# Kernel tuning notes

Measured on AMD Instinct MI355X. Metric: run time of the kernel, lower is better.

The kernel has to match this reference:

```python
import jax, jax.numpy as jnp
import numpy as np


def setup_inputs() -> dict:
    key = jax.random.key(0)
    k1, k2, k3, k4, k5 = jax.random.split(key, 5)
    B, S, D, F, E = 4, 4096, 1024, 2048, 8
    top_k = 2
    num_tokens = B * S
    capacity = max(int(num_tokens / E * 1.25), 4)  # 2560
    scale = 0.02
    return {
        "x": jax.random.normal(k1, (B, S, D), dtype=jnp.float32),
        "gate_w": jax.random.normal(k2, (D, E), dtype=jnp.float32) * scale,
        "w_gate": jax.random.normal(k3, (E, D, F), dtype=jnp.float32) * scale,
        "w_up": jax.random.normal(k4, (E, D, F), dtype=jnp.float32) * scale,
        "w_down": jax.random.normal(k5, (E, F, D), dtype=jnp.float32) * scale,
        "num_experts": E,
        "top_k": top_k,
        "capacity": capacity,
    }


AUX_LOSS_WEIGHT = 0.01


def reference(x, gate_w, w_gate, w_up, w_down, num_experts, top_k, capacity):
    B, S, D = x.shape
    N = B * S
    x_flat = x.reshape(N, D)

    # ---- Router ----
    logits = x_flat @ gate_w                      # [N, E]
    probs = jax.nn.softmax(logits, axis=-1)
    weights, indices = jax.lax.top_k(probs, top_k)  # [N, K]
    weights = weights / jnp.sum(weights, axis=-1, keepdims=True)

    # ---- Capacity-based dispatch ----
    indices_flat = indices.reshape(-1)            # [N*K]
    x_rep = jnp.repeat(x_flat, top_k, axis=0)     # [N*K, D]
    expert_mask = jax.nn.one_hot(indices_flat, num_experts, dtype=jnp.int32)  # [N*K, E]
    token_priority = jnp.cumsum(expert_mask, axis=0) * expert_mask
    token_rank = jnp.sum(token_priority, axis=1)  # [N*K], 1-based rank within expert
    valid = (token_rank > 0) & (token_rank <= capacity)
    gather_idx = indices_flat * capacity + (token_rank - 1)  # [N*K]

    total_slots = num_experts * capacity
    # drop-mode scatter: invalid rows are sent out-of-bounds and dropped
    safe_idx = jnp.where(valid, gather_idx, total_slots)
    dispatched = jnp.zeros((total_slots, D), dtype=x.dtype)
    dispatched = dispatched.at[safe_idx].set(x_rep, mode="drop")
    dispatched = dispatched.reshape(num_experts, capacity, D)  # [E, C, D]

    # ---- Fused experts (grouped BMM, SwiGLU) ----
    gate = jnp.einsum("ecd,edf->ecf", dispatched, w_gate)
    up = jnp.einsum("ecd,edf->ecf", dispatched, w_up)
    hidden = jax.nn.silu(gate) * up
    expert_out = jnp.einsum("ecf,efd->ecd", hidden, w_down)
    expert_out_flat = expert_out.reshape(total_slots, D)

    # ---- Combine (row-aligned gather; dropped tokens contribute zero) ----
    gathered = expert_out_flat[jnp.clip(gather_idx, 0, total_slots - 1)]
    combined = jnp.where(valid[:, None], gathered, jnp.zeros((), dtype=x.dtype))
    combined = combined.reshape(N, top_k, D)
    output = jnp.sum(combined * weights[:, :, None], axis=1)  # [N, D]

    # ---- Aux load-balance loss ----
    mask = jax.nn.one_hot(indices, num_experts, dtype=jnp.float32).sum(axis=1)  # [N, E]
    f = mask.sum(axis=0) / (N * top_k + 1e-9)
    P = probs.mean(axis=0)
    aux_loss = num_experts * jnp.sum(f * P) * AUX_LOSS_WEIGHT

    return output.reshape(B, S, D), aux_loss
```

## Files before the change

### kernel.cpp

```cpp
#include <hip/hip_runtime.h>
#include <stdint.h>

#define N_TOK 16384
#define DIM   1024
#define NEXP  8
#define FF    2048
#define CAP   2560
#define NSLOT (NEXP*CAP)

using f32x4  = __attribute__((ext_vector_type(4))) float;
using bf16x8 = __attribute__((ext_vector_type(8))) short;

__device__ __forceinline__ unsigned short f2bf(float f){
  union { float f; unsigned u; } c; c.f = f;
  unsigned u = c.u + 0x7FFFu + ((c.u >> 16) & 1u);
  return (unsigned short)(u >> 16);
}
__device__ __forceinline__ float bf2f(unsigned short h){
  union { unsigned u; float f; } c; c.u = ((unsigned)h) << 16; return c.f;
}

__device__ __forceinline__ void gld16(const unsigned short* g, unsigned short* l){
  __builtin_amdgcn_global_load_lds((__attribute__((address_space(1))) void*)(void*)g,
                                   (__attribute__((address_space(3))) void*)l,
                                   16, 0, 0);
}

#define HBAR __builtin_amdgcn_s_barrier()
#define LG0  asm volatile("s_waitcnt lgkmcnt(0)" ::: "memory")

__global__ __launch_bounds__(256) void k_router(
    const float* __restrict__ x, const float* __restrict__ gate_w,
    float* __restrict__ probs, int* __restrict__ topidx, float* __restrict__ topw)
{
  __shared__ float gwT[NEXP][DIM];
  int tid = threadIdx.x;
  for (int i = tid; i < DIM*NEXP; i += 256) gwT[i & 7][i >> 3] = gate_w[i];
  __syncthreads();
  int wave = tid >> 6, lane = tid & 63;
  int t = blockIdx.x * 4 + wave;
  const float* xr = x + (size_t)t * DIM;
  double acc[NEXP];
  #pragma unroll
  for (int e = 0; e < NEXP; e++) acc[e] = 0.0;
  for (int j = 0; j < DIM/64; j++){
    double xv = (double)xr[lane + 64*j];
    #pragma unroll
    for (int e = 0; e < NEXP; e++) acc[e] += xv * (double)gwT[e][lane + 64*j];
  }
  #pragma unroll
  for (int off = 32; off >= 1; off >>= 1){
    #pragma unroll
    for (int e = 0; e < NEXP; e++) acc[e] += __shfl_xor(acc[e], off, 64);
  }
  if (lane == 0){
    double m = acc[0];
    #pragma unroll
    for (int e = 1; e < NEXP; e++) m = fmax(m, acc[e]);
    double p[NEXP], Z = 0.0;
    #pragma unroll
    for (int e = 0; e < NEXP; e++){ p[e] = exp(acc[e] - m); Z += p[e]; }
    double invZ = 1.0 / Z;
    #pragma unroll
    for (int e = 0; e < NEXP; e++){ p[e] *= invZ; probs[t*NEXP + e] = (float)p[e]; }
    int i0 = 0; double p0 = p[0];
    #pragma unroll
    for (int e = 1; e < NEXP; e++) if (p[e] > p0){ p0 = p[e]; i0 = e; }
    int i1 = (i0 == 0) ? 1 : 0; double p1 = p[i1];
    #pragma unroll
    for (int e = 0; e < NEXP; e++) if (e != i0 && p[e] > p1){ p1 = p[e]; i1 = e; }
    double s = p0 + p1;
    topidx[t*2+0] = i0; topidx[t*2+1] = i1;
    topw [t*2+0] = (float)(p0/s); topw[t*2+1] = (float)(p1/s);
  }
}

__global__ __launch_bounds__(1024) void k_scan(
    const int* __restrict__ topidx,
    int* __restrict__ slot_token, int* __restrict__ tok_slots,
    int* __restrict__ counts_total)
{
  __shared__ int sc[1024][NEXP];
  const int t = threadIdx.x;
  const int base_i = t * 32;
  int ids[32];
  #pragma unroll
  for (int j = 0; j < 32; j++) ids[j] = topidx[base_i + j];
  int b[NEXP];
  #pragma unroll
  for (int e = 0; e < NEXP; e++) b[e] = 0;
  #pragma unroll
  for (int j = 0; j < 32; j++){
    #pragma unroll
    for (int e = 0; e < NEXP; e++) if (ids[j] == e) b[e]++;
  }
  #pragma unroll
  for (int e = 0; e < NEXP; e++) sc[t][e] = b[e];
  __syncthreads();
  for (int off = 1; off < 1024; off <<= 1){
    int tmp[NEXP];
    #pragma unroll
    for (int e = 0; e < NEXP; e++) tmp[e] = (t >= off) ? sc[t-off][e] : 0;
    __syncthreads();
    #pragma unroll
    for (int e = 0; e < NEXP; e++) sc[t][e] += tmp[e];
    __syncthreads();
  }
  int myb[NEXP];
  #pragma unroll
  for (int e = 0; e < NEXP; e++) myb[e] = sc[t][e] - b[e];
  if (t == 1023){
    #pragma unroll
    for (int e = 0; e < NEXP; e++) counts_total[e] = sc[1023][e];
  }
  #pragma unroll
  for (int j = 0; j < 32; j++){
    int slot = -1;
    #pragma unroll
    for (int e = 0; e < NEXP; e++){
      if (ids[j] == e){
        int r = myb[e]; myb[e] = r + 1;
        if (r < CAP){
          slot = e*CAP + r;
          slot_token[slot] = (base_i + j) >> 1;
        }
      }
    }
    tok_slots[base_i + j] = slot;
  }
}

template<int MODE>
__global__ __launch_bounds__(256) void k_tcv(
    const float* __restrict__ in, unsigned short* __restrict__ out,
    int R, int C, size_t estride)
{
  __shared__ float tt[64][65];
  const int e  = blockIdx.z;
  const float* ine = in + (size_t)e * R * C;
  unsigned short* oute = out + (size_t)e * estride;
  const int c0 = blockIdx.x * 64, r0 = blockIdx.y * 64;
  const int tid = threadIdx.x;
  #pragma unroll
  for (int i = 0; i < 4; i++){
    int idx = i*256 + tid;
    int row = idx >> 4, c4 = idx & 15;
    float4 v = *(const float4*)(ine + (size_t)(r0 + row)*C + c0 + c4*4);
    tt[c4*4+0][row] = v.x; tt[c4*4+1][row] = v.y;
    tt[c4*4+2][row] = v.z; tt[c4*4+3][row] = v.w;
  }
  __syncthreads();
  #pragma unroll
  for (int i = 0; i < 2; i++){
    int cl = i*32 + (tid >> 3);
    int rs = (tid & 7) * 8;
    int c  = c0 + cl;
    int orow = (MODE == 0) ? ((c>>4)*32 + (c&15))
             : (MODE == 1) ? ((c>>4)*32 + 16 + (c&15))
             : c;
    unsigned long long pk0 = 0, pk1 = 0;
    #pragma unroll
    for (int j = 0; j < 4; j++) pk0 |= (unsigned long long)f2bf(tt[cl][rs+j]) << (16*j);
    #pragma unroll
    for (int j = 0; j < 4; j++) pk1 |= (unsigned long long)f2bf(tt[cl][rs+4+j]) << (16*j);
    unsigned long long* dst = (unsigned long long*)(oute + (size_t)orow*R + r0 + rs);
    dst[0] = pk0; dst[1] = pk1;
  }
}

__global__ __launch_bounds__(256) void k_gather(
    const float* __restrict__ x, const int* __restrict__ slot_token,
    unsigned short* __restrict__ disp)
{
  const int s = blockIdx.x;
  const int t = slot_token[s];
  const int tid = threadIdx.x;
  unsigned long long pk = 0ull;
  if (t >= 0){
    float4 v = *(const float4*)(x + (size_t)t*DIM + tid*4);
    pk =  (unsigned long long)f2bf(v.x)
       | ((unsigned long long)f2bf(v.y) << 16)
       | ((unsigned long long)f2bf(v.z) << 32)
       | ((unsigned long long)f2bf(v.w) << 48);
  }
  *(unsigned long long*)(disp + (size_t)s*DIM + tid*4) = pk;
}

__device__ __forceinline__ void stg(const unsigned short* gsrc, int ldg,
                                    unsigned short* Lh, int wave, int lane){
  const int sl = (lane & 3) ^ ((lane >> 3) & 3);
  #pragma unroll
  for (int j = 0; j < 2; j++){
    int bi = wave*2 + j;
    gld16(gsrc + (size_t)(bi*16 + (lane >> 2))*ldg + sl*8, Lh + bi*512);
  }
}
__device__ __forceinline__ bf16x8 frd(const unsigned short* Lh, int r, int g){
  return *(const bf16x8*)(Lh + r*32 + (((g ^ ((r >> 1) & 3))) << 3));
}
template<int MG>
__device__ __forceinline__ void mm16(f32x4 (&acc)[8][4], const bf16x8 (&a)[4], const bf16x8 (&b)[4]){
  #pragma unroll
  for (int i = 0; i < 4; i++)
    #pragma unroll
    for (int n = 0; n < 4; n++)
      acc[MG*4+i][n] = __builtin_amdgcn_mfma_f32_16x16x32_bf16(a[i], b[n], acc[MG*4+i][n], 0, 0, 0);
}

#define HALF_STEP(RS, DOSTG, VMW, ASRC, BSRC)                                   \
  {                                                                             \
    unsigned short* LA = lds + (RS)*16384;                                      \
    unsigned short* LB = LA + 8192;                                             \
    unsigned short* NS = lds + (((RS)+3)&3)*16384;                              \
    bf16x8 a[4], b[4];                                                          \
    _Pragma("unroll")                                                           \
    for (int i = 0; i < 4; i++) a[i] = frd(LA, wr*128 + i*16 + l15, g);         \
    _Pragma("unroll")                                                           \
    for (int n = 0; n < 4; n++) b[n] = frd(LB, wc*64 + n*16 + l15, g);          \
    if (DOSTG) stg(ASRC, LDG, NS, wave, lane);                                  \
    HBAR; LG0;                                                                  \
    __builtin_amdgcn_s_setprio(1);  mm16<0>(acc, a, b);                         \
    __builtin_amdgcn_s_setprio(0);                                              \
    HBAR;                                                                       \
    _Pragma("unroll")                                                           \
    for (int i = 0; i < 4; i++) a[i] = frd(LA, wr*128 + (4+i)*16 + l15, g);     \
    if (DOSTG) stg(BSRC, LDG, NS + 8192, wave, lane);                           \
    HBAR; LG0;                                                                  \
    __builtin_amdgcn_s_setprio(1);  mm16<1>(acc, a, b);                         \
    __builtin_amdgcn_s_setprio(0);                                              \
    if ((VMW) == 4) { asm volatile("s_waitcnt vmcnt(4)" ::: "memory"); }        \
    else if ((VMW) == 0) { asm volatile("s_waitcnt vmcnt(0)" ::: "memory"); }   \
    HBAR;                                                                       \
  }

template<int KDIM, int LDG, int EPI>
__global__ __launch_bounds__(512, 2) void k_gemm8(
    const unsigned short* __restrict__ A,
    const unsigned short* __restrict__ B,
    unsigned short* __restrict__ Out0,
    unsigned short* __restrict__ Out1)
{
  constexpr int NH    = KDIM / 32;
  constexpr int BROWS = (EPI == 1) ? 2*FF : DIM;
  constexpr int LDO   = (EPI == 1) ? FF : DIM;
  __shared__ unsigned short lds[65536];
  const int id = blockIdx.x;
  const int e  = id & 7;
  int t  = id >> 3;
  int ks = 0;
  if (EPI == 2){ ks = t & 1; t >>= 1; }
  const int mt = t % 10, nt = t / 10;
  const int m0 = mt*256, n0 = nt*256;
  const unsigned short* Ab = A + ((size_t)e*CAP   + m0) * LDG + (size_t)ks*KDIM;
  const unsigned short* Bb = B + ((size_t)e*BROWS + n0) * LDG + (size_t)ks*KDIM;
  const int tid = threadIdx.x, wave = tid >> 6, lane = tid & 63;
  const int wr = wave >> 2, wc = wave & 3;
  const int g = lane >> 4, l15 = lane & 15;

  f32x4 acc[8][4];
  const f32x4 z4 = {0.f,0.f,0.f,0.f};
  #pragma unroll
  for (int i = 0; i < 8; i++)
    #pragma unroll
    for (int n = 0; n < 4; n++) acc[i][n] = z4;

  stg(Ab,      LDG, lds + 0*16384,        wave, lane);
  stg(Bb,      LDG, lds + 0*16384 + 8192, wave, lane);
  stg(Ab + 32, LDG, lds + 1*16384,        wave, lane);
  stg(Bb + 32, LDG, lds + 1*16384 + 8192, wave, lane);
  stg(Ab + 64, LDG, lds + 2*16384,        wave, lane);
  stg(Bb + 64, LDG, lds + 2*16384 + 8192, wave, lane);
  asm volatile("s_waitcnt vmcnt(4)" ::: "memory");
  HBAR;

  for (int h = 0; h + 8 <= NH; h += 4){
    HALF_STEP(0, true, -1, Ab + (size_t)(h+3)*32, Bb + (size_t)(h+3)*32);
    HALF_STEP(1, true,  4, Ab + (size_t)(h+4)*32, Bb + (size_t)(h+4)*32);
    HALF_STEP(2, true, -1, Ab + (size_t)(h+5)*32, Bb + (size_t)(h+5)*32);
    HALF_STEP(3, true,  4, Ab + (size_t)(h+6)*32, Bb + (size_t)(h+6)*32);
  }
  HALF_STEP(0, true, -1, Ab + (size_t)(NH-1)*32, Bb + (size_t)(NH-1)*32);
  HALF_STEP(1, false, 0, Ab, Bb);
  HALF_STEP(2, false, -1, Ab, Bb);
  HALF_STEP(3, false, -1, Ab, Bb);

  if (EPI == 1){
    unsigned short* H = Out0 + ((size_t)e*CAP + m0 + wr*128) * (size_t)LDO;
    const int hc0 = (n0 + wc*64) >> 1;
    #pragma unroll
    for (int mf = 0; mf < 8; mf++)
      #pragma unroll
      for (int q = 0; q < 4; q++){
        int r = mf*16 + g*4 + q;
        #pragma unroll
        for (int p = 0; p < 2; p++){
          float gg = acc[mf][2*p][q], uu = acc[mf][2*p+1][q];
          float h = gg / (1.f + __expf(-gg)) * uu;
          H[(size_t)r*LDO + hc0 + p*16 + l15] = f2bf(h);
        }
      }
  } else {
    unsigned short* P = (ks ? Out1 : Out0);
    unsigned short* O = P + ((size_t)e*CAP + m0 + wr*128) * (size_t)LDO + n0 + wc*64;
    #pragma unroll
    for (int mf = 0; mf < 8; mf++)
      #pragma unroll
      for (int q = 0; q < 4; q++){
        int r = mf*16 + g*4 + q;
        #pragma unroll
        for (int n = 0; n < 4; n++)
          O[(size_t)r*LDO + n*16 + l15] = f2bf(acc[mf][n][q]);
      }
  }
}

__global__ __launch_bounds__(256) void k_combine(
    const unsigned short* __restrict__ P0, const unsigned short* __restrict__ P1,
    const int* __restrict__ tok_slots, const float* __restrict__ topw,
    float* __restrict__ out)
{
  const int t = blockIdx.x*2 + (threadIdx.x >> 7);
  const int tid = threadIdx.x & 127;
  const int s0 = tok_slots[t*2+0], s1 = tok_slots[t*2+1];
  const float w0 = topw[t*2+0], w1 = topw[t*2+1];
  float r[8];
  #pragma unroll
  for (int j = 0; j < 8; j++) r[j] = 0.f;
  if (s0 >= 0){
    bf16x8 v0 = *(const bf16x8*)(P0 + (size_t)s0*DIM + tid*8);
    bf16x8 v1 = *(const bf16x8*)(P1 + (size_t)s0*DIM + tid*8);
    #pragma unroll
    for (int j = 0; j < 8; j++)
      r[j] += w0 * (bf2f((unsigned short)v0[j]) + bf2f((unsigned short)v1[j]));
  }
  if (s1 >= 0){
    bf16x8 v0 = *(const bf16x8*)(P0 + (size_t)s1*DIM + tid*8);
    bf16x8 v1 = *(const bf16x8*)(P1 + (size_t)s1*DIM + tid*8);
    #pragma unroll
    for (int j = 0; j < 8; j++)
      r[j] += w1 * (bf2f((unsigned short)v0[j]) + bf2f((unsigned short)v1[j]));
  }
  float4* o = (float4*)(out + (size_t)t*DIM + tid*8);
  o[0] = make_float4(r[0], r[1], r[2], r[3]);
  o[1] = make_float4(r[4], r[5], r[6], r[7]);
}

__global__ __launch_bounds__(256) void k_aux(
    const float* __restrict__ probs, const int* __restrict__ counts_total,
    float* __restrict__ aux_out)
{
  const int tid = threadIdx.x;
  float pe[NEXP];
  #pragma unroll
  for (int e = 0; e < NEXP; e++) pe[e] = 0.f;
  for (int i = tid; i < N_TOK; i += 256){
    #pragma unroll
    for (int e = 0; e < NEXP; e++) pe[e] += probs[i*NEXP + e];
  }
  #pragma unroll
  for (int off = 32; off >= 1; off >>= 1){
    #pragma unroll
    for (int e = 0; e < NEXP; e++) pe[e] += __shfl_xor(pe[e], off, 64);
  }
  __shared__ float part[4][NEXP];
  const int wave = tid >> 6, lane = tid & 63;
  if (lane == 0){
    #pragma unroll
    for (int e = 0; e < NEXP; e++) part[wave][e] = pe[e];
  }
  __syncthreads();
  if (tid == 0){
    float aux = 0.f;
    for (int e = 0; e < NEXP; e++){
      float P = (part[0][e] + part[1][e] + part[2][e] + part[3][e]) / (float)N_TOK;
      float f = (float)counts_total[e] / ((float)(N_TOK*2) + 1e-9f);
      aux += f * P;
    }
    aux_out[0] = (float)NEXP * aux * 0.01f;
  }
}

extern "C" void kernel_launch(void* const* d_in, const int* in_sizes, int n_in,
                              void* d_out, int out_size, void* d_ws, size_t ws_size,
                              hipStream_t stream)
{
  const float* x      = (const float*)d_in[0];
  const float* gate_w = (const float*)d_in[1];
  const float* w_gate = (const float*)d_in[2];
  const float* w_up   = (const float*)d_in[3];
  const float* w_down = (const float*)d_in[4];
  float* out = (float*)d_out;

  uint8_t* ws = (uint8_t*)d_ws;
  float* probs        = (float*)ws;             ws += (size_t)N_TOK*NEXP*4;
  int*   topidx       = (int*)ws;               ws += (size_t)N_TOK*2*4;
  float* topw         = (float*)ws;             ws += (size_t)N_TOK*2*4;
  int*   slot_token   = (int*)ws;               ws += (size_t)NSLOT*4;
  int*   tok_slots    = (int*)ws;               ws += (size_t)N_TOK*2*4;
  int*   counts_total = (int*)ws;               ws += 256;
  unsigned short* disp   = (unsigned short*)ws; ws += (size_t)NSLOT*DIM*2;
  unsigned short* hidden = (unsigned short*)ws; ws += (size_t)NSLOT*FF*2;
  unsigned short* B1     = (unsigned short*)ws; ws += (size_t)NEXP*2*FF*DIM*2;
  unsigned short* wdT    = (unsigned short*)ws; ws += (size_t)NEXP*DIM*FF*2;
  size_t need = (size_t)(ws - (uint8_t*)d_ws);
  if (ws_size < need) return;
  unsigned short* P0 = disp;
  unsigned short* P1 = B1;

  hipMemsetAsync(slot_token, 0xFF, (size_t)NSLOT * sizeof(int), stream);

  k_router<<<N_TOK/4, 256, 0, stream>>>(x, gate_w, probs, topidx, topw);
  k_scan<<<1, 1024, 0, stream>>>(topidx, slot_token, tok_slots, counts_total);
  k_tcv<0><<<dim3(FF/64, DIM/64, NEXP), 256, 0, stream>>>(w_gate, B1, DIM, FF, (size_t)2*FF*DIM);
  k_tcv<1><<<dim3(FF/64, DIM/64, NEXP), 256, 0, stream>>>(w_up,   B1, DIM, FF, (size_t)2*FF*DIM);
  k_tcv<2><<<dim3(DIM/64, FF/64, NEXP), 256, 0, stream>>>(w_down, wdT, FF, DIM, (size_t)DIM*FF);
  k_gather<<<NSLOT, 256, 0, stream>>>(x, slot_token, disp);
  k_gemm8<DIM, DIM, 1><<<1280, 512, 0, stream>>>(disp, B1, hidden, nullptr);
  k_gemm8<DIM, FF, 2><<<640, 512, 0, stream>>>(hidden, wdT, P0, P1);
  k_combine<<<N_TOK/2, 256, 0, stream>>>(P0, P1, tok_slots, topw, out);
  k_aux<<<1, 256, 0, stream>>>(probs, counts_total, out + (size_t)N_TOK*DIM);
}
```

Measured before the change: 501.6 us.

## Restructure GEMM main loop, merge weight-convert launches, fold aux loss into scan

Replaces the unrolled HALF_STEP GEMM pipeline with a per-stage loop. Each iteration issues both A and B prefetches, reads the whole A fragment set and prefetches the next stage's B fragments, then runs all 32 MFMAs per stage with fewer barriers. It also merges the three weight transpose/convert launches into one grid and moves the aux-loss reduction into the scan kernel, removing a launch. The fewer barriers and larger MFMA bursts may raise register pressure or change how well loads overlap with compute.

Result: faster. 483.4 us (-3.6%).

```diff
diff --git a/kernel.cpp b/kernel.cpp
--- a/kernel.cpp
+++ b/kernel.cpp
@@ -28,6 +28,7 @@
 
 #define HBAR __builtin_amdgcn_s_barrier()
 #define LG0  asm volatile("s_waitcnt lgkmcnt(0)" ::: "memory")
+#define SBAR0 __builtin_amdgcn_sched_barrier(0)
 
 __global__ __launch_bounds__(256) void k_router(
     const float* __restrict__ x, const float* __restrict__ gate_w,
@@ -76,9 +77,9 @@
 }
 
 __global__ __launch_bounds__(1024) void k_scan(
-    const int* __restrict__ topidx,
+    const int* __restrict__ topidx, const float* __restrict__ probs,
     int* __restrict__ slot_token, int* __restrict__ tok_slots,
-    int* __restrict__ counts_total)
+    float* __restrict__ aux_out)
 {
   __shared__ int sc[1024][NEXP];
   const int t = threadIdx.x;
@@ -109,10 +110,9 @@
   int myb[NEXP];
   #pragma unroll
   for (int e = 0; e < NEXP; e++) myb[e] = sc[t][e] - b[e];
-  if (t == 1023){
-    #pragma unroll
-    for (int e = 0; e < NEXP; e++) counts_total[e] = sc[1023][e];
-  }
+  int cnt[NEXP];
+  #pragma unroll
+  for (int e = 0; e < NEXP; e++) cnt[e] = sc[1023][e];
   #pragma unroll
   for (int j = 0; j < 32; j++){
     int slot = -1;
@@ -128,24 +128,66 @@
     }
     tok_slots[base_i + j] = slot;
   }
-}
-
-template<int MODE>
-__global__ __launch_bounds__(256) void k_tcv(
-    const float* __restrict__ in, unsigned short* __restrict__ out,
-    int R, int C, size_t estride)
+  __syncthreads();
+  float pe[NEXP];
+  #pragma unroll
+  for (int e = 0; e < NEXP; e++) pe[e] = 0.f;
+  for (int i = t; i < N_TOK; i += 1024){
+    const float4* pr = (const float4*)(probs + i*NEXP);
+    float4 v0 = pr[0], v1 = pr[1];
+    pe[0] += v0.x; pe[1] += v0.y; pe[2] += v0.z; pe[3] += v0.w;
+    pe[4] += v1.x; pe[5] += v1.y; pe[6] += v1.z; pe[7] += v1.w;
+  }
+  #pragma unroll
+  for (int off = 32; off >= 1; off >>= 1){
+    #pragma unroll
+    for (int e = 0; e < NEXP; e++) pe[e] += __shfl_xor(pe[e], off, 64);
+  }
+  __syncthreads();
+  float* scf = (float*)&sc[0][0];
+  const int wv = t >> 6, ln = t & 63;
+  if (ln == 0){
+    #pragma unroll
+    for (int e = 0; e < NEXP; e++) scf[wv*NEXP + e] = pe[e];
+  }
+  __syncthreads();
+  if (t == 0){
+    float aux = 0.f;
+    #pragma unroll
+    for (int e = 0; e < NEXP; e++){
+      float P = 0.f;
+      for (int w = 0; w < 16; w++) P += scf[w*NEXP + e];
+      P /= (float)N_TOK;
+      float f = (float)cnt[e] / ((float)(N_TOK*2) + 1e-9f);
+      aux += f * P;
+    }
+    aux_out[0] = (float)NEXP * aux * 0.01f;
+  }
+}
+
+__global__ __launch_bounds__(256) void k_tcv_all(
+    const float* __restrict__ wg, const float* __restrict__ wu, const float* __restrict__ wd,
+    unsigned short* __restrict__ B1, unsigned short* __restrict__ wdT)
 {
   __shared__ float tt[64][65];
-  const int e  = blockIdx.z;
-  const float* ine = in + (size_t)e * R * C;
-  unsigned short* oute = out + (size_t)e * estride;
-  const int c0 = blockIdx.x * 64, r0 = blockIdx.y * 64;
+  const int z = blockIdx.z, mode = z >> 3, e = z & 7;
+  const float* in; unsigned short* out; int R, C, ct, rt;
+  if (mode < 2){
+    in  = (mode == 0 ? wg : wu) + (size_t)e * DIM * FF;
+    out = B1 + (size_t)e * 2 * FF * DIM;
+    R = DIM; C = FF; ct = blockIdx.x; rt = blockIdx.y;
+  } else {
+    in  = wd + (size_t)e * FF * DIM;
+    out = wdT + (size_t)e * DIM * FF;
+    R = FF; C = DIM; ct = blockIdx.y; rt = blockIdx.x;
+  }
+  const int c0 = ct * 64, r0 = rt * 64;
   const int tid = threadIdx.x;
   #pragma unroll
   for (int i = 0; i < 4; i++){
     int idx = i*256 + tid;
     int row = idx >> 4, c4 = idx & 15;
-    float4 v = *(const float4*)(ine + (size_t)(r0 + row)*C + c0 + c4*4);
+    float4 v = *(const float4*)(in + (size_t)(r0 + row)*C + c0 + c4*4);
     tt[c4*4+0][row] = v.x; tt[c4*4+1][row] = v.y;
     tt[c4*4+2][row] = v.z; tt[c4*4+3][row] = v.w;
   }
@@ -155,15 +197,15 @@
     int cl = i*32 + (tid >> 3);
     int rs = (tid & 7) * 8;
     int c  = c0 + cl;
-    int orow = (MODE == 0) ? ((c>>4)*32 + (c&15))
-             : (MODE == 1) ? ((c>>4)*32 + 16 + (c&15))
+    int orow = (mode == 0) ? ((c>>4)*32 + (c&15))
+             : (mode == 1) ? ((c>>4)*32 + 16 + (c&15))
              : c;
     unsigned long long pk0 = 0, pk1 = 0;
     #pragma unroll
     for (int j = 0; j < 4; j++) pk0 |= (unsigned long long)f2bf(tt[cl][rs+j]) << (16*j);
     #pragma unroll
     for (int j = 0; j < 4; j++) pk1 |= (unsigned long long)f2bf(tt[cl][rs+4+j]) << (16*j);
-    unsigned long long* dst = (unsigned long long*)(oute + (size_t)orow*R + r0 + rs);
+    unsigned long long* dst = (unsigned long long*)(out + (size_t)orow*R + r0 + rs);
     dst[0] = pk0; dst[1] = pk1;
   }
 }
@@ -206,32 +248,6 @@
     for (int n = 0; n < 4; n++)
       acc[MG*4+i][n] = __builtin_amdgcn_mfma_f32_16x16x32_bf16(a[i], b[n], acc[MG*4+i][n], 0, 0, 0);
 }
-
-#define HALF_STEP(RS, DOSTG, VMW, ASRC, BSRC)                                   \
-  {                                                                             \
-    unsigned short* LA = lds + (RS)*16384;                                      \
-    unsigned short* LB = LA + 8192;                                             \
-    unsigned short* NS = lds + (((RS)+3)&3)*16384;                              \
-    bf16x8 a[4], b[4];                                                          \
-    _Pragma("unroll")                                                           \
-    for (int i = 0; i < 4; i++) a[i] = frd(LA, wr*128 + i*16 + l15, g);         \
-    _Pragma("unroll")                                                           \
-    for (int n = 0; n < 4; n++) b[n] = frd(LB, wc*64 + n*16 + l15, g);          \
-    if (DOSTG) stg(ASRC, LDG, NS, wave, lane);                                  \
-    HBAR; LG0;                                                                  \
-    __builtin_amdgcn_s_setprio(1);  mm16<0>(acc, a, b);                         \
-    __builtin_amdgcn_s_setprio(0);                                              \
-    HBAR;                                                                       \
-    _Pragma("unroll")                                                           \
-    for (int i = 0; i < 4; i++) a[i] = frd(LA, wr*128 + (4+i)*16 + l15, g);     \
-    if (DOSTG) stg(BSRC, LDG, NS + 8192, wave, lane);                           \
-    HBAR; LG0;                                                                  \
-    __builtin_amdgcn_s_setprio(1);  mm16<1>(acc, a, b);                         \
-    __builtin_amdgcn_s_setprio(0);                                              \
-    if ((VMW) == 4) { asm volatile("s_waitcnt vmcnt(4)" ::: "memory"); }        \
-    else if ((VMW) == 0) { asm volatile("s_waitcnt vmcnt(0)" ::: "memory"); }   \
-    HBAR;                                                                       \
-  }
 
 template<int KDIM, int LDG, int EPI>
 __global__ __launch_bounds__(512, 2) void k_gemm8(
@@ -272,17 +288,42 @@
   stg(Bb + 64, LDG, lds + 2*16384 + 8192, wave, lane);
   asm volatile("s_waitcnt vmcnt(4)" ::: "memory");
   HBAR;
-
-  for (int h = 0; h + 8 <= NH; h += 4){
-    HALF_STEP(0, true, -1, Ab + (size_t)(h+3)*32, Bb + (size_t)(h+3)*32);
-    HALF_STEP(1, true,  4, Ab + (size_t)(h+4)*32, Bb + (size_t)(h+4)*32);
-    HALF_STEP(2, true, -1, Ab + (size_t)(h+5)*32, Bb + (size_t)(h+5)*32);
-    HALF_STEP(3, true,  4, Ab + (size_t)(h+6)*32, Bb + (size_t)(h+6)*32);
-  }
-  HALF_STEP(0, true, -1, Ab + (size_t)(NH-1)*32, Bb + (size_t)(NH-1)*32);
-  HALF_STEP(1, false, 0, Ab, Bb);
-  HALF_STEP(2, false, -1, Ab, Bb);
-  HALF_STEP(3, false, -1, Ab, Bb);
+  SBAR0;
+  bf16x8 bh[4];
+  #pragma unroll
+  for (int n = 0; n < 4; n++) bh[n] = frd(lds + 8192, wc*64 + n*16 + l15, g);
+
+  for (int h = 0; h < NH; ++h){
+    unsigned short* LA = lds + (h & 3)*16384;
+    if (h + 3 < NH){
+      unsigned short* NS = lds + ((h+3) & 3)*16384;
+      stg(Ab + (size_t)(h+3)*32, LDG, NS,        wave, lane);
+      stg(Bb + (size_t)(h+3)*32, LDG, NS + 8192, wave, lane);
+    }
+    bf16x8 a[4], a2[4], bn[4];
+    #pragma unroll
+    for (int i = 0; i < 4; i++) a[i]  = frd(LA, wr*128 + i*16 + l15, g);
+    #pragma unroll
+    for (int i = 0; i < 4; i++) a2[i] = frd(LA, wr*128 + (4+i)*16 + l15, g);
+    if (h + 1 < NH){
+      unsigned short* NL = lds + ((h+1) & 3)*16384 + 8192;
+      #pragma unroll
+      for (int n = 0; n < 4; n++) bn[n] = frd(NL, wc*64 + n*16 + l15, g);
+    }
+    LG0; SBAR0;
+    __builtin_amdgcn_s_setprio(1);
+    mm16<0>(acc, a, bh);
+    mm16<1>(acc, a2, bh);
+    __builtin_amdgcn_s_setprio(0);
+    if (h + 1 < NH){
+      #pragma unroll
+      for (int n = 0; n < 4; n++) bh[n] = bn[n];
+    }
+    if (h <= NH-4)      { asm volatile("s_waitcnt vmcnt(4)" ::: "memory"); }
+    else if (h == NH-3) { asm volatile("s_waitcnt vmcnt(0)" ::: "memory"); }
+    HBAR;
+    SBAR0;
+  }
 
   if (EPI == 1){
     unsigned short* H = Out0 + ((size_t)e*CAP + m0 + wr*128) * (size_t)LDO;
@@ -345,41 +386,6 @@
   o[1] = make_float4(r[4], r[5], r[6], r[7]);
 }
 
-__global__ __launch_bounds__(256) void k_aux(
-    const float* __restrict__ probs, const int* __restrict__ counts_total,
-    float* __restrict__ aux_out)
-{
-  const int tid = threadIdx.x;
-  float pe[NEXP];
-  #pragma unroll
-  for (int e = 0; e < NEXP; e++) pe[e] = 0.f;
-  for (int i = tid; i < N_TOK; i += 256){
-    #pragma unroll
-    for (int e = 0; e < NEXP; e++) pe[e] += probs[i*NEXP + e];
-  }
-  #pragma unroll
-  for (int off = 32; off >= 1; off >>= 1){
-    #pragma unroll
-    for (int e = 0; e < NEXP; e++) pe[e] += __shfl_xor(pe[e], off, 64);
-  }
-  __shared__ float part[4][NEXP];
-  const int wave = tid >> 6, lane = tid & 63;
-  if (lane == 0){
-    #pragma unroll
-    for (int e = 0; e < NEXP; e++) part[wave][e] = pe[e];
-  }
-  __syncthreads();
-  if (tid == 0){
-    float aux = 0.f;
-    for (int e = 0; e < NEXP; e++){
-      float P = (part[0][e] + part[1][e] + part[2][e] + part[3][e]) / (float)N_TOK;
-      float f = (float)counts_total[e] / ((float)(N_TOK*2) + 1e-9f);
-      aux += f * P;
-    }
-    aux_out[0] = (float)NEXP * aux * 0.01f;
-  }
-}
-
 extern "C" void kernel_launch(void* const* d_in, const int* in_sizes, int n_in,
                               void* d_out, int out_size, void* d_ws, size_t ws_size,
                               hipStream_t stream)
@@ -397,7 +403,7 @@
   float* topw         = (float*)ws;             ws += (size_t)N_TOK*2*4;
   int*   slot_token   = (int*)ws;               ws += (size_t)NSLOT*4;
   int*   tok_slots    = (int*)ws;               ws += (size_t)N_TOK*2*4;
-  int*   counts_total = (int*)ws;               ws += 256;
+  int*   counts_total = (int*)ws;               ws += 256;  (void)counts_total;
   unsigned short* disp   = (unsigned short*)ws; ws += (size_t)NSLOT*DIM*2;
   unsigned short* hidden = (unsigned short*)ws; ws += (size_t)NSLOT*FF*2;
   unsigned short* B1     = (unsigned short*)ws; ws += (size_t)NEXP*2*FF*DIM*2;
@@ -410,13 +416,11 @@
   hipMemsetAsync(slot_token, 0xFF, (size_t)NSLOT * sizeof(int), stream);
 
   k_router<<<N_TOK/4, 256, 0, stream>>>(x, gate_w, probs, topidx, topw);
-  k_scan<<<1, 1024, 0, stream>>>(topidx, slot_token, tok_slots, counts_total);
-  k_tcv<0><<<dim3(FF/64, DIM/64, NEXP), 256, 0, stream>>>(w_gate, B1, DIM, FF, (size_t)2*FF*DIM);
-  k_tcv<1><<<dim3(FF/64, DIM/64, NEXP), 256, 0, stream>>>(w_up,   B1, DIM, FF, (size_t)2*FF*DIM);
-  k_tcv<2><<<dim3(DIM/64, FF/64, NEXP), 256, 0, stream>>>(w_down, wdT, FF, DIM, (size_t)DIM*FF);
+  k_scan<<<1, 1024, 0, stream>>>(topidx, probs, slot_token, tok_slots,
+                                 out + (size_t)N_TOK*DIM);
+  k_tcv_all<<<dim3(32, 16, 24), 256, 0, stream>>>(w_gate, w_up, w_down, B1, wdT);
   k_gather<<<NSLOT, 256, 0, stream>>>(x, slot_token, disp);
   k_gemm8<DIM, DIM, 1><<<1280, 512, 0, stream>>>(disp, B1, hidden, nullptr);
   k_gemm8<DIM, FF, 2><<<640, 512, 0, stream>>>(hidden, wdT, P0, P1);
   k_combine<<<N_TOK/2, 256, 0, stream>>>(P0, P1, tok_slots, topw, out);
-  k_aux<<<1, 256, 0, stream>>>(probs, counts_total, out + (size_t)N_TOK*DIM);
-}
+}
```
